# Optimization experiments

Measured on AMD Instinct MI355X. Metric: run time of the kernel, lower is better.

Reference implementation:

```python
import jax, jax.numpy as jnp
import numpy as np

EMBED_DIM = 512
NUM_HEADS = 8
HEAD_DIM = EMBED_DIM // NUM_HEADS
SCALE = HEAD_DIM ** -0.5
B, N = 4, 2048


def _linear_params(key, fan_in, fan_out):
    kw, kb = jax.random.split(key)
    bound = 1.0 / np.sqrt(fan_in)
    W = jax.random.uniform(kw, (fan_out, fan_in), minval=-bound, maxval=bound, dtype=jnp.float32)
    b = jax.random.uniform(kb, (fan_out,), minval=-bound, maxval=bound, dtype=jnp.float32)
    return W, b


def setup_inputs() -> dict:
    key = jax.random.key(0)
    ks = jax.random.split(key, 7)
    query = jax.random.normal(ks[0], (B, N, EMBED_DIM), dtype=jnp.float32)
    k_in = jax.random.normal(ks[1], (B, N, EMBED_DIM), dtype=jnp.float32)
    v_in = jax.random.normal(ks[2], (B, N, EMBED_DIM), dtype=jnp.float32)
    Wq, bq = _linear_params(ks[3], EMBED_DIM, EMBED_DIM)
    Wk, bk = _linear_params(ks[4], EMBED_DIM, EMBED_DIM)
    Wv, bv = _linear_params(ks[5], EMBED_DIM, EMBED_DIM)
    Wo, bo = _linear_params(ks[6], EMBED_DIM, EMBED_DIM)
    return {
        "query": query, "key": k_in, "value": v_in,
        "Wq": Wq, "bq": bq, "Wk": Wk, "bk": bk,
        "Wv": Wv, "bv": bv, "Wo": Wo, "bo": bo,
    }


def reference(query, key, value, Wq, bq, Wk, bk, Wv, bv, Wo, bo):
    Bq, Nq, _ = query.shape
    # projections: (B, S, E) x (E, E)^T + b
    q = (query @ Wq.T + bq).reshape(Bq, Nq, NUM_HEADS, HEAD_DIM).transpose(0, 2, 1, 3)  # bhnd
    k = (key @ Wk.T + bk).reshape(Bq, -1, NUM_HEADS, HEAD_DIM).transpose(0, 2, 1, 3)    # bhmd
    v = (value @ Wv.T + bv).reshape(Bq, -1, NUM_HEADS, HEAD_DIM).transpose(0, 2, 1, 3)  # bhmd
    attn = jnp.einsum('bhnd,bhmd->bhnm', q, k) * SCALE
    attn = jax.nn.softmax(attn, axis=-1)
    x = jnp.einsum('bhnm,bhmd->bhnd', attn, v)
    x = x.transpose(0, 2, 1, 3).reshape(Bq, Nq, EMBED_DIM)
    return x @ Wo.T + bo
```

## Files before the change

kernel.cpp:

```cpp
#include <hip/hip_runtime.h>
#include <stdint.h>

#define NX (8192*512)
#define NW (512*512)

typedef __bf16 bf16x8 __attribute__((ext_vector_type(8)));
typedef float  f32x4  __attribute__((ext_vector_type(4)));
typedef float  f32x16 __attribute__((ext_vector_type(16)));

__device__ __forceinline__ unsigned short f2bf(float f){
  unsigned u = __builtin_bit_cast(unsigned, f);
  u += 0x7FFFu + ((u >> 16) & 1u);
  return (unsigned short)(u >> 16);
}

__device__ __forceinline__ f32x4 mfma16(bf16x8 a, bf16x8 b, f32x4 c){
  return __builtin_amdgcn_mfma_f32_16x16x32_bf16(a, b, c, 0, 0, 0);
}
__device__ __forceinline__ f32x16 mfma32(bf16x8 a, bf16x8 b, f32x16 c){
  return __builtin_amdgcn_mfma_f32_32x32x16_bf16(a, b, c, 0, 0, 0);
}

__device__ __forceinline__ void gload_lds16(const void* g, void* l){
  __builtin_amdgcn_global_load_lds((const __attribute__((address_space(1))) void*)g,
                                   (__attribute__((address_space(3))) void*)l, 16, 0, 0);
}

#define VMCNT(n) asm volatile("s_waitcnt vmcnt(" #n ")" ::: "memory")

__global__ void convert_all(const float* __restrict__ q, const float* __restrict__ k,
                            const float* __restrict__ v, const float* __restrict__ wq,
                            const float* __restrict__ wk, const float* __restrict__ wv,
                            const float* __restrict__ wo, unsigned short* __restrict__ dst)
{
  const long total4 = (3L*NX + 4L*NW) / 4;
  for (long i = (long)blockIdx.x*blockDim.x + threadIdx.x; i < total4; i += (long)gridDim.x*blockDim.x){
    long e = i*4;
    const float* src; long off;
    if (e < NX)            { src = q;  off = e; }
    else if (e < 2L*NX)    { src = k;  off = e - NX; }
    else if (e < 3L*NX)    { src = v;  off = e - 2L*NX; }
    else {
      long w = e - 3L*NX; int wi = (int)(w / NW); off = w - (long)wi*NW;
      src = (wi==0) ? wq : (wi==1) ? wk : (wi==2) ? wv : wo;
    }
    float4 f = *(const float4*)(src + off);
    ushort4 o; o.x=f2bf(f.x); o.y=f2bf(f.y); o.z=f2bf(f.z); o.w=f2bf(f.w);
    *(ushort4*)(dst + e) = o;
  }
}

struct GArg {
  const unsigned short* A;
  const unsigned short* B;
  const float* bias;
  void* C;
  float scale;
  int mode;
};

__global__ __launch_bounds__(256) void gemm_bt(GArg g0, GArg g1, GArg g2)
{
  GArg g = (blockIdx.z==0) ? g0 : (blockIdx.z==1) ? g1 : g2;
  __shared__ __attribute__((aligned(16))) unsigned char lds[65536];
  const int tid  = threadIdx.x;
  const int lane = tid & 63;
  const int wid  = tid >> 6;
  const int wr = wid >> 1, wc = wid & 1;
  const int m0 = blockIdx.y * 128;
  const int n0 = blockIdx.x * 128;

  f32x4 acc[4][4];
  #pragma unroll
  for (int s=0;s<4;s++)
    #pragma unroll
    for (int t=0;t<4;t++) acc[s][t] = (f32x4){0.f,0.f,0.f,0.f};

  auto stage = [&](int kt, int buf){
    int Lb = tid*16;
    #pragma unroll
    for (int i=0;i<4;i++){
      int L = Lb + i*4096;
      int row = L >> 7;
      int innerS = (L & 127) ^ ((row & 7) << 4);
      gload_lds16(g.A + (size_t)(m0+row)*512 + kt*64 + (innerS>>1), lds + buf*16384 + L);
    }
    #pragma unroll
    for (int i=0;i<4;i++){
      int L = Lb + i*4096;
      int row = L >> 7;
      int innerS = (L & 127) ^ ((row & 7) << 4);
      gload_lds16(g.B + (size_t)(n0+row)*512 + kt*64 + (innerS>>1), lds + 32768 + buf*16384 + L);
    }
  };

  stage(0, 0);
  VMCNT(0);
  __syncthreads();

  for (int kt=0; kt<8; kt++){
    int cur = kt & 1;
    if (kt < 7) stage(kt+1, cur^1);
    const unsigned char* LA = lds + cur*16384;
    const unsigned char* LB = lds + 32768 + cur*16384;
    #pragma unroll
    for (int ks=0; ks<2; ks++){
      bf16x8 af[4], bfr[4];
      #pragma unroll
      for (int s=0;s<4;s++){
        int row = wr*64 + s*16 + (lane & 15);
        int inner = (ks*32 + (lane>>4)*8)*2;
        af[s] = *(const bf16x8*)(LA + row*128 + (inner ^ ((row&7)<<4)));
      }
      #pragma unroll
      for (int t=0;t<4;t++){
        int row = wc*64 + t*16 + (lane & 15);
        int inner = (ks*32 + (lane>>4)*8)*2;
        bfr[t] = *(const bf16x8*)(LB + row*128 + (inner ^ ((row&7)<<4)));
      }
      #pragma unroll
      for (int s=0;s<4;s++)
        #pragma unroll
        for (int t=0;t<4;t++)
          acc[s][t] = mfma16(af[s], bfr[t], acc[s][t]);
    }
    VMCNT(0);
    __syncthreads();
  }

  if (g.mode == 2){
    float* C = (float*)g.C;
    #pragma unroll
    for (int t=0;t<4;t++){
      int col = n0 + wc*64 + t*16 + (lane&15);
      float bv = g.bias[col];
      #pragma unroll
      for (int s=0;s<4;s++){
        #pragma unroll
        for (int r=0;r<4;r++){
          int row = m0 + wr*64 + s*16 + (lane>>4)*4 + r;
          C[(size_t)row*512 + col] = acc[s][t][r] + bv;
        }
      }
    }
  } else if (g.mode == 0){
    unsigned short* C = (unsigned short*)g.C;
    #pragma unroll
    for (int t=0;t<4;t++){
      int col = n0 + wc*64 + t*16 + (lane&15);
      float bv = g.bias[col];
      #pragma unroll
      for (int s=0;s<4;s++){
        #pragma unroll
        for (int r=0;r<4;r++){
          int row = m0 + wr*64 + s*16 + (lane>>4)*4 + r;
          C[(size_t)row*512 + col] = f2bf((acc[s][t][r] + bv) * g.scale);
        }
      }
    }
  } else {
    __syncthreads();
    unsigned short* T = (unsigned short*)lds;
    #pragma unroll
    for (int s=0;s<4;s++){
      #pragma unroll
      for (int t=0;t<4;t++){
        int col  = wc*64 + t*16 + (lane&15);
        int rowb = wr*64 + s*16 + (lane>>4)*4;
        float bv = g.bias[n0+col];
        ushort4 pk;
        pk.x = f2bf(acc[s][t][0] + bv);
        pk.y = f2bf(acc[s][t][1] + bv);
        pk.z = f2bf(acc[s][t][2] + bv);
        pk.w = f2bf(acc[s][t][3] + bv);
        *(ushort4*)(T + col*136 + rowb) = pk;
      }
    }
    __syncthreads();
    unsigned short* Vt = (unsigned short*)g.C;
    int col = tid >> 1, half = tid & 1;
    int gcol = n0 + col;
    int hh = gcol >> 6, d = gcol & 63;
    int b = m0 >> 11, ms = m0 & 2047;
    unsigned short* dst = Vt + (((size_t)(b*8+hh)*64 + d)*2048 + ms + half*64);
    const unsigned short* srcT = T + col*136 + half*64;
    #pragma unroll
    for (int j=0;j<8;j++)
      *(int4*)(dst + j*8) = *(const int4*)(srcT + j*8);
  }
}

__global__ __launch_bounds__(512, 4) void attn_kernel(
    const unsigned short* __restrict__ Qs,
    const unsigned short* __restrict__ Kb,
    const unsigned short* __restrict__ Vt,
    unsigned short* __restrict__ AO)
{
  __shared__ __attribute__((aligned(16))) unsigned char lds[55296];
  const int tid = threadIdx.x, lane = tid & 63, wid = tid >> 6;
  const int half = wid >> 2, widh = wid & 3, tid_h = tid & 255;
  const int hi = lane >> 5, lq = lane & 31;

  const int flat = blockIdx.y*16 + blockIdx.x;
  const int work = (flat & 7)*64 + (flat >> 3);
  const int bh = work >> 4, qtile = work & 15;
  const int b = bh >> 3, h = bh & 7;
  const int q0 = qtile*128 + widh*32;

  const unsigned short* KbaseH = Kb + (size_t)b*2048*512 + h*64 + (size_t)half*1024*512;
  const unsigned short* VbaseH = Vt + (size_t)bh*64*2048 + half*1024;
  unsigned char* KLDS = lds + half*12288;
  unsigned char* VLDS = lds + 24576 + half*15360;

  bf16x8 qf[4];
  #pragma unroll
  for (int c=0;c<4;c++)
    qf[c] = *(const bf16x8*)(Qs + (size_t)(b*2048 + q0 + lq)*512 + h*64 + c*16 + hi*8);

  int koff[4];
  #pragma unroll
  for (int c=0;c<4;c++)
    koff[c] = lq*128 + ((c*32 + hi*16) ^ ((lq & 7) << 4));
  int voff[2][2];
  #pragma unroll
  for (int dh=0;dh<2;dh++)
    #pragma unroll
    for (int cb=0;cb<2;cb++)
      voff[dh][cb] = (dh*32 + lq)*80 + cb*32 + hi*16;

  const int sL = tid_h >> 3;
  const int sI = (tid_h & 7) * 16;
  const int sArow = (sL&3) + 4*((sL>>3)&1) + 8*((sL>>2)&1) + 16*((sL>>4)&1);
  const int sSrc = ((sI ^ ((sL & 7) << 4)) >> 1);
  const int vrow = widh*16 + (lane & 15);
  const int vpart = lane >> 4;

  auto stageK = [&](int t, int buf){
    gload_lds16(KbaseH + (size_t)(t*32 + sArow)*512 + sSrc, KLDS + buf*4096 + tid_h*16);
  };
  auto loadV = [&](int t){
    return *(const uint4*)(VbaseH + (size_t)vrow*2048 + t*32 + vpart*8);
  };
  auto writeV = [&](int buf, uint4 v){
    *(uint4*)(VLDS + buf*5120 + vrow*80 + vpart*16) = v;
  };

  f32x16 o[2];
  o[0] = (f32x16)(0.f); o[1] = (f32x16)(0.f);
  float m_run = -1e30f, l_run = 0.f;

  auto qkt = [&](int buf) -> f32x16 {
    const unsigned char* KL = KLDS + buf*4096;
    f32x16 S = (f32x16)(0.f);
    #pragma unroll
    for (int c=0;c<4;c++){
      bf16x8 kf = *(const bf16x8*)(KL + koff[c]);
      S = mfma32(kf, qf[c], S);
    }
    return S;
  };

  auto finish = [&](f32x16 S, int vbuf){
    const unsigned char* VL = VLDS + vbuf*5120;
    float a0 = fmaxf(fmaxf(S[0],S[1]),S[2]);
    float a1 = fmaxf(fmaxf(S[3],S[4]),S[5]);
    float a2 = fmaxf(fmaxf(S[6],S[7]),S[8]);
    float a3 = fmaxf(fmaxf(S[9],S[10]),S[11]);
    float a4 = fmaxf(fmaxf(S[12],S[13]),S[14]);
    float mt = fmaxf(fmaxf(fmaxf(a0,a1),a2), fmaxf(fmaxf(a3,a4),S[15]));
    mt = fmaxf(mt, __shfl_xor(mt, 32));

    if (!__all(mt <= m_run + 11.5415603f)){
      float mn = fmaxf(m_run, mt);
      float corr = exp2f(m_run - mn);
      l_run *= corr;
      m_run = mn;
      #pragma unroll
      for (int r=0;r<16;r++){ o[0][r] *= corr; o[1][r] *= corr; }
    }

    float p[16];
    #pragma unroll
    for (int r=0;r<16;r++) p[r] = exp2f(S[r] - m_run);

    float rs = (((p[0]+p[1])+(p[2]+p[3]))+((p[4]+p[5])+(p[6]+p[7])))
             + (((p[8]+p[9])+(p[10]+p[11]))+((p[12]+p[13])+(p[14]+p[15])));
    rs += __shfl_xor(rs, 32);
    l_run += rs;

    bf16x8 pf0, pf1;
    #pragma unroll
    for (int j=0;j<8;j++){ pf0[j] = (__bf16)p[j]; pf1[j] = (__bf16)p[8+j]; }

    #pragma unroll
    for (int dh=0;dh<2;dh++){
      bf16x8 v0 = *(const bf16x8*)(VL + voff[dh][0]);
      o[dh] = mfma32(v0, pf0, o[dh]);
      bf16x8 v1 = *(const bf16x8*)(VL + voff[dh][1]);
      o[dh] = mfma32(v1, pf1, o[dh]);
    }
  };

  stageK(0, 0); stageK(1, 1);
  uint4 VgA = loadV(0);
  VMCNT(0); writeV(0, VgA);
  __syncthreads();
  VgA = loadV(1); stageK(2, 2);
  f32x16 S_a = qkt(0);
  VMCNT(1); writeV(1, VgA);
  __syncthreads();

  for (int t=0; t<30; t+=2){
    VgA = loadV(t+2);
    stageK(t+3, t%3);
    f32x16 S_b = qkt((t+1)%3);
    finish(S_a, t%3);
    VMCNT(1); writeV((t+2)%3, VgA);
    __syncthreads();
    VgA = loadV(t+3);
    if (t < 28) stageK(t+4, (t+1)%3);
    S_a = qkt((t+2)%3);
    finish(S_b, (t+1)%3);
    VMCNT(1); writeV((t+3)%3, VgA);
    __syncthreads();
  }
  {
    f32x16 S_b = qkt(1);
    finish(S_a, 0);
    finish(S_b, 1);
  }

  __syncthreads();
  float* mo = (float*)lds + widh*2048;
  float* ml = (float*)(lds + 53248);
  if (half == 1){
    #pragma unroll
    for (int dh=0; dh<2; dh++)
      #pragma unroll
      for (int r=0; r<16; r++){
        int d = dh*32 + (r&3) + 8*(r>>2) + 4*hi;
        mo[d*32 + lq] = o[dh][r];
      }
    if (lane < 32){
      ml[(widh*32 + lq)*2]     = m_run;
      ml[(widh*32 + lq)*2 + 1] = l_run;
    }
  }
  __syncthreads();
  if (half == 0){
    float m1 = ml[(widh*32 + lq)*2];
    float l1 = ml[(widh*32 + lq)*2 + 1];
    float mm = fmaxf(m_run, m1);
    float c0 = exp2f(m_run - mm);
    float c1 = exp2f(m1 - mm);
    float inv = 1.0f / (l_run*c0 + l1*c1);
    float ca = c0*inv, cb = c1*inv;
    unsigned short* dst = AO + (size_t)(b*2048 + q0 + lq)*512 + h*64;
    #pragma unroll
    for (int dh=0; dh<2; dh++){
      #pragma unroll
      for (int g2=0; g2<4; g2++){
        int d0 = dh*32 + g2*8 + hi*4;
        ushort4 pk;
        pk.x = f2bf(o[dh][g2*4+0]*ca + mo[(d0+0)*32+lq]*cb);
        pk.y = f2bf(o[dh][g2*4+1]*ca + mo[(d0+1)*32+lq]*cb);
        pk.z = f2bf(o[dh][g2*4+2]*ca + mo[(d0+2)*32+lq]*cb);
        pk.w = f2bf(o[dh][g2*4+3]*ca + mo[(d0+3)*32+lq]*cb);
        *(ushort4*)(dst + dh*32 + g2*8 + hi*4) = pk;
      }
    }
  }
}

extern "C" void kernel_launch(void* const* d_in, const int* in_sizes, int n_in,
                              void* d_out, int out_size, void* d_ws, size_t ws_size,
                              hipStream_t stream)
{
  const float* q  = (const float*)d_in[0];
  const float* k  = (const float*)d_in[1];
  const float* v  = (const float*)d_in[2];
  const float* Wq = (const float*)d_in[3];
  const float* bq = (const float*)d_in[4];
  const float* Wk = (const float*)d_in[5];
  const float* bk = (const float*)d_in[6];
  const float* Wv = (const float*)d_in[7];
  const float* bv = (const float*)d_in[8];
  const float* Wo = (const float*)d_in[9];
  const float* bo = (const float*)d_in[10];

  unsigned short* X   = (unsigned short*)d_ws;
  unsigned short* Xq  = X;
  unsigned short* Xk  = X + NX;
  unsigned short* Xv  = X + 2*(size_t)NX;
  unsigned short* WqB = X + 3*(size_t)NX;
  unsigned short* WkB = WqB + NW;
  unsigned short* WvB = WqB + 2*(size_t)NW;
  unsigned short* WoB = WqB + 3*(size_t)NW;
  unsigned short* QS  = WqB + 4*(size_t)NW;
  unsigned short* KB  = QS + NX;
  unsigned short* VT  = KB + NX;
  unsigned short* AO  = VT + NX;

  convert_all<<<dim3(2048), dim3(256), 0, stream>>>(q, k, v, Wq, Wk, Wv, Wo, X);

  GArg gq{Xq, WqB, bq, (void*)QS, 0.180336878f, 0};
  GArg gk{Xk, WkB, bk, (void*)KB, 1.0f,   0};
  GArg gv{Xv, WvB, bv, (void*)VT, 1.0f,   1};
  gemm_bt<<<dim3(4, 64, 3), dim3(256), 0, stream>>>(gq, gk, gv);

  attn_kernel<<<dim3(16, 32), dim3(512), 0, stream>>>(QS, KB, VT, AO);

  GArg go{AO, WoB, bo, d_out, 1.0f, 2};
  gemm_bt<<<dim3(4, 64, 1), dim3(256), 0, stream>>>(go, go, go);
}
```

Baseline: 111.4 us.

## Fuse fp32-to-bf16 activation conversion into QKV GEMM A-tile staging

Removes the separate pass that converted the q/k/v activations to bf16. The QKV GEMM now loads fp32 A tiles into registers, converts them, and writes them swizzled into LDS while the MFMA work on the current buffer proceeds. Only the weights are still converted in a small separate kernel. The attention kernel's __syncthreads are also replaced with an explicit lgkmcnt wait plus s_barrier. This saves a full write and reread of the bf16 activation copies, in exchange for more register pressure and reading twice as many A bytes from global memory inside the GEMM. Each column tile rereads the same fp32 rows, so the A traffic repeats across the four column blocks.

```diff
diff --git a/kernel.cpp b/kernel.cpp
--- a/kernel.cpp
+++ b/kernel.cpp
@@ -27,31 +27,23 @@
 }
 
 #define VMCNT(n) asm volatile("s_waitcnt vmcnt(" #n ")" ::: "memory")
-
-__global__ void convert_all(const float* __restrict__ q, const float* __restrict__ k,
-                            const float* __restrict__ v, const float* __restrict__ wq,
-                            const float* __restrict__ wk, const float* __restrict__ wv,
-                            const float* __restrict__ wo, unsigned short* __restrict__ dst)
+#define BARRIER() asm volatile("s_waitcnt lgkmcnt(0)\n\ts_barrier" ::: "memory")
+
+__global__ void convert_w(const float* __restrict__ wq, const float* __restrict__ wk,
+                          const float* __restrict__ wv, const float* __restrict__ wo,
+                          unsigned short* __restrict__ dst)
 {
-  const long total4 = (3L*NX + 4L*NW) / 4;
-  for (long i = (long)blockIdx.x*blockDim.x + threadIdx.x; i < total4; i += (long)gridDim.x*blockDim.x){
-    long e = i*4;
-    const float* src; long off;
-    if (e < NX)            { src = q;  off = e; }
-    else if (e < 2L*NX)    { src = k;  off = e - NX; }
-    else if (e < 3L*NX)    { src = v;  off = e - 2L*NX; }
-    else {
-      long w = e - 3L*NX; int wi = (int)(w / NW); off = w - (long)wi*NW;
-      src = (wi==0) ? wq : (wi==1) ? wk : (wi==2) ? wv : wo;
-    }
-    float4 f = *(const float4*)(src + off);
-    ushort4 o; o.x=f2bf(f.x); o.y=f2bf(f.y); o.z=f2bf(f.z); o.w=f2bf(f.w);
-    *(ushort4*)(dst + e) = o;
-  }
-}
-
-struct GArg {
-  const unsigned short* A;
+  long i = (long)blockIdx.x*blockDim.x + threadIdx.x;
+  long e = i*4;
+  int wi = (int)(e / NW); long off = e - (long)wi*NW;
+  const float* src = (wi==0) ? wq : (wi==1) ? wk : (wi==2) ? wv : wo;
+  float4 f = *(const float4*)(src + off);
+  ushort4 o; o.x=f2bf(f.x); o.y=f2bf(f.y); o.z=f2bf(f.z); o.w=f2bf(f.w);
+  *(ushort4*)(dst + e) = o;
+}
+
+struct GArgF {
+  const float* A;
   const unsigned short* B;
   const float* bias;
   void* C;
@@ -59,9 +51,9 @@
   int mode;
 };
 
-__global__ __launch_bounds__(256) void gemm_bt(GArg g0, GArg g1, GArg g2)
+__global__ __launch_bounds__(256) void gemm_qkv(GArgF g0, GArgF g1, GArgF g2)
 {
-  GArg g = (blockIdx.z==0) ? g0 : (blockIdx.z==1) ? g1 : g2;
+  GArgF g = (blockIdx.z==0) ? g0 : (blockIdx.z==1) ? g1 : g2;
   __shared__ __attribute__((aligned(16))) unsigned char lds[65536];
   const int tid  = threadIdx.x;
   const int lane = tid & 63;
@@ -69,6 +61,7 @@
   const int wr = wid >> 1, wc = wid & 1;
   const int m0 = blockIdx.y * 128;
   const int n0 = blockIdx.x * 128;
+  const int arow = tid >> 1, ahalf = tid & 1;
 
   f32x4 acc[4][4];
   #pragma unroll
@@ -76,15 +69,26 @@
     #pragma unroll
     for (int t=0;t<4;t++) acc[s][t] = (f32x4){0.f,0.f,0.f,0.f};
 
-  auto stage = [&](int kt, int buf){
+  float4 abuf[8];
+  auto loadA = [&](int kt){
+    const float* src = g.A + (size_t)(m0+arow)*512 + kt*64 + ahalf*32;
+    #pragma unroll
+    for (int j=0;j<8;j++) abuf[j] = *(const float4*)(src + j*4);
+  };
+  auto writeA = [&](int buf){
+    unsigned char* dst = lds + buf*16384 + arow*128;
+    #pragma unroll
+    for (int j=0;j<4;j++){
+      int4 w;
+      w.x = (unsigned)f2bf(abuf[2*j].x)   | ((unsigned)f2bf(abuf[2*j].y)<<16);
+      w.y = (unsigned)f2bf(abuf[2*j].z)   | ((unsigned)f2bf(abuf[2*j].w)<<16);
+      w.z = (unsigned)f2bf(abuf[2*j+1].x) | ((unsigned)f2bf(abuf[2*j+1].y)<<16);
+      w.w = (unsigned)f2bf(abuf[2*j+1].z) | ((unsigned)f2bf(abuf[2*j+1].w)<<16);
+      *(int4*)(dst + ((ahalf*64 + j*16) ^ ((arow&7)<<4))) = w;
+    }
+  };
+  auto stageB = [&](int kt, int buf){
     int Lb = tid*16;
-    #pragma unroll
-    for (int i=0;i<4;i++){
-      int L = Lb + i*4096;
-      int row = L >> 7;
-      int innerS = (L & 127) ^ ((row & 7) << 4);
-      gload_lds16(g.A + (size_t)(m0+row)*512 + kt*64 + (innerS>>1), lds + buf*16384 + L);
-    }
     #pragma unroll
     for (int i=0;i<4;i++){
       int L = Lb + i*4096;
@@ -94,13 +98,14 @@
     }
   };
 
-  stage(0, 0);
+  loadA(0); stageB(0, 0);
+  writeA(0);
   VMCNT(0);
   __syncthreads();
 
   for (int kt=0; kt<8; kt++){
     int cur = kt & 1;
-    if (kt < 7) stage(kt+1, cur^1);
+    if (kt < 7){ loadA(kt+1); stageB(kt+1, cur^1); }
     const unsigned char* LA = lds + cur*16384;
     const unsigned char* LB = lds + 32768 + cur*16384;
     #pragma unroll
@@ -124,26 +129,12 @@
         for (int t=0;t<4;t++)
           acc[s][t] = mfma16(af[s], bfr[t], acc[s][t]);
     }
+    if (kt < 7) writeA(cur^1);
     VMCNT(0);
     __syncthreads();
   }
 
-  if (g.mode == 2){
-    float* C = (float*)g.C;
-    #pragma unroll
-    for (int t=0;t<4;t++){
-      int col = n0 + wc*64 + t*16 + (lane&15);
-      float bv = g.bias[col];
-      #pragma unroll
-      for (int s=0;s<4;s++){
-        #pragma unroll
-        for (int r=0;r<4;r++){
-          int row = m0 + wr*64 + s*16 + (lane>>4)*4 + r;
-          C[(size_t)row*512 + col] = acc[s][t][r] + bv;
-        }
-      }
-    }
-  } else if (g.mode == 0){
+  if (g.mode == 0){
     unsigned short* C = (unsigned short*)g.C;
     #pragma unroll
     for (int t=0;t<4;t++){
@@ -190,6 +181,97 @@
   }
 }
 
+struct GArg {
+  const unsigned short* A;
+  const unsigned short* B;
+  const float* bias;
+  void* C;
+};
+
+__global__ __launch_bounds__(256) void gemm_bt(GArg g)
+{
+  __shared__ __attribute__((aligned(16))) unsigned char lds[65536];
+  const int tid  = threadIdx.x;
+  const int lane = tid & 63;
+  const int wid  = tid >> 6;
+  const int wr = wid >> 1, wc = wid & 1;
+  const int m0 = blockIdx.y * 128;
+  const int n0 = blockIdx.x * 128;
+
+  f32x4 acc[4][4];
+  #pragma unroll
+  for (int s=0;s<4;s++)
+    #pragma unroll
+    for (int t=0;t<4;t++) acc[s][t] = (f32x4){0.f,0.f,0.f,0.f};
+
+  auto stage = [&](int kt, int buf){
+    int Lb = tid*16;
+    #pragma unroll
+    for (int i=0;i<4;i++){
+      int L = Lb + i*4096;
+      int row = L >> 7;
+      int innerS = (L & 127) ^ ((row & 7) << 4);
+      gload_lds16(g.A + (size_t)(m0+row)*512 + kt*64 + (innerS>>1), lds + buf*16384 + L);
+    }
+    #pragma unroll
+    for (int i=0;i<4;i++){
+      int L = Lb + i*4096;
+      int row = L >> 7;
+      int innerS = (L & 127) ^ ((row & 7) << 4);
+      gload_lds16(g.B + (size_t)(n0+row)*512 + kt*64 + (innerS>>1), lds + 32768 + buf*16384 + L);
+    }
+  };
+
+  stage(0, 0);
+  VMCNT(0);
+  __syncthreads();
+
+  for (int kt=0; kt<8; kt++){
+    int cur = kt & 1;
+    if (kt < 7) stage(kt+1, cur^1);
+    const unsigned char* LA = lds + cur*16384;
+    const unsigned char* LB = lds + 32768 + cur*16384;
+    #pragma unroll
+    for (int ks=0; ks<2; ks++){
+      bf16x8 af[4], bfr[4];
+      #pragma unroll
+      for (int s=0;s<4;s++){
+        int row = wr*64 + s*16 + (lane & 15);
+        int inner = (ks*32 + (lane>>4)*8)*2;
+        af[s] = *(const bf16x8*)(LA + row*128 + (inner ^ ((row&7)<<4)));
+      }
+      #pragma unroll
+      for (int t=0;t<4;t++){
+        int row = wc*64 + t*16 + (lane & 15);
+        int inner = (ks*32 + (lane>>4)*8)*2;
+        bfr[t] = *(const bf16x8*)(LB + row*128 + (inner ^ ((row&7)<<4)));
+      }
+      #pragma unroll
+      for (int s=0;s<4;s++)
+        #pragma unroll
+        for (int t=0;t<4;t++)
+          acc[s][t] = mfma16(af[s], bfr[t], acc[s][t]);
+    }
+    VMCNT(0);
+    __syncthreads();
+  }
+
+  float* C = (float*)g.C;
+  #pragma unroll
+  for (int t=0;t<4;t++){
+    int col = n0 + wc*64 + t*16 + (lane&15);
+    float bv = g.bias[col];
+    #pragma unroll
+    for (int s=0;s<4;s++){
+      #pragma unroll
+      for (int r=0;r<4;r++){
+        int row = m0 + wr*64 + s*16 + (lane>>4)*4 + r;
+        C[(size_t)row*512 + col] = acc[s][t][r] + bv;
+      }
+    }
+  }
+}
+
 __global__ __launch_bounds__(512, 4) void attn_kernel(
     const unsigned short* __restrict__ Qs,
     const unsigned short* __restrict__ Kb,
@@ -304,11 +386,11 @@
   stageK(0, 0); stageK(1, 1);
   uint4 VgA = loadV(0);
   VMCNT(0); writeV(0, VgA);
-  __syncthreads();
+  BARRIER();
   VgA = loadV(1); stageK(2, 2);
   f32x16 S_a = qkt(0);
   VMCNT(1); writeV(1, VgA);
-  __syncthreads();
+  BARRIER();
 
   for (int t=0; t<30; t+=2){
     VgA = loadV(t+2);
@@ -316,13 +398,13 @@
     f32x16 S_b = qkt((t+1)%3);
     finish(S_a, t%3);
     VMCNT(1); writeV((t+2)%3, VgA);
-    __syncthreads();
+    BARRIER();
     VgA = loadV(t+3);
     if (t < 28) stageK(t+4, (t+1)%3);
     S_a = qkt((t+2)%3);
     finish(S_b, (t+1)%3);
     VMCNT(1); writeV((t+3)%3, VgA);
-    __syncthreads();
+    BARRIER();
   }
   {
     f32x16 S_b = qkt(1);
@@ -389,10 +471,7 @@
   const float* bo = (const float*)d_in[10];
 
   unsigned short* X   = (unsigned short*)d_ws;
-  unsigned short* Xq  = X;
-  unsigned short* Xk  = X + NX;
-  unsigned short* Xv  = X + 2*(size_t)NX;
-  unsigned short* WqB = X + 3*(size_t)NX;
+  unsigned short* WqB = X;
   unsigned short* WkB = WqB + NW;
   unsigned short* WvB = WqB + 2*(size_t)NW;
   unsigned short* WoB = WqB + 3*(size_t)NW;
@@ -401,15 +480,15 @@
   unsigned short* VT  = KB + NX;
   unsigned short* AO  = VT + NX;
 
-  convert_all<<<dim3(2048), dim3(256), 0, stream>>>(q, k, v, Wq, Wk, Wv, Wo, X);
-
-  GArg gq{Xq, WqB, bq, (void*)QS, 0.180336878f, 0};
-  GArg gk{Xk, WkB, bk, (void*)KB, 1.0f,   0};
-  GArg gv{Xv, WvB, bv, (void*)VT, 1.0f,   1};
-  gemm_bt<<<dim3(4, 64, 3), dim3(256), 0, stream>>>(gq, gk, gv);
+  convert_w<<<dim3(1024), dim3(256), 0, stream>>>(Wq, Wk, Wv, Wo, X);
+
+  GArgF gq{q, WqB, bq, (void*)QS, 0.180336878f, 0};
+  GArgF gk{k, WkB, bk, (void*)KB, 1.0f, 0};
+  GArgF gv{v, WvB, bv, (void*)VT, 1.0f, 1};
+  gemm_qkv<<<dim3(4, 64, 3), dim3(256), 0, stream>>>(gq, gk, gv);
 
   attn_kernel<<<dim3(16, 32), dim3(512), 0, stream>>>(QS, KB, VT, AO);
 
-  GArg go{AO, WoB, bo, d_out, 1.0f, 2};
-  gemm_bt<<<dim3(4, 64, 1), dim3(256), 0, stream>>>(go, go, go);
-}
+  GArg go{AO, WoB, bo, d_out};
+  gemm_bt<<<dim3(4, 64), dim3(256), 0, stream>>>(go);
+}
```

Result: slower. 128.3 us (+15.2%).
